# Kernel tuning notes

Hardware: AMD Instinct MI355X
Metric: run time of the kernel (lower is better)

Reference implementation:

```python
import jax, jax.numpy as jnp
import numpy as np

N_PTS = 2000   # n: number of Z1 samples (rows of K_Z1Z1)
Z_PTS = 2000   # z: number of Z2 samples (cols of K_Z1Z2 / gammas)
A_SAMP = 1000  # a: number of alpha samples
D = 8          # d: treatment dimension


def setup_inputs() -> dict:
    key = jax.random.key(0)
    ks = jax.random.split(key, 8)
    M = jax.random.normal(ks[0], (N_PTS, D), jnp.float32)
    N = jax.random.normal(ks[1], (N_PTS, D), jnp.float32)
    X = (M + N) / 2  # initial_X in the torch module (the nn.Parameter)
    # PSD kernel matrix so the ridge solve is well conditioned
    A = jax.random.normal(ks[2], (N_PTS, N_PTS), jnp.float32)
    K_Z1Z1 = (A @ A.T) / N_PTS
    K_Z1Z2 = jax.random.normal(ks[3], (N_PTS, Z_PTS), jnp.float32) * 0.1
    gamma_MN = jax.random.normal(ks[4], (N_PTS, Z_PTS), jnp.float32) * 0.01
    # offset keeps the complex denominator exps @ gamma_N away from zero
    gamma_N = jax.random.normal(ks[5], (N_PTS, Z_PTS), jnp.float32) * 0.01 + 1.0 / N_PTS
    alpha_samples = jax.random.normal(ks[6], (A_SAMP, D), jnp.float32)
    log_lambda_X = jnp.zeros((1,), jnp.float32)  # log(lambda_N) with lambda_N = 1.0
    return {
        "M": M, "N": N, "X": X, "log_lambda_X": log_lambda_X,
        "K_Z1Z1": K_Z1Z1, "K_Z1Z2": K_Z1Z2,
        "gamma_MN": gamma_MN, "gamma_N": gamma_N,
        "alpha_samples": alpha_samples,
    }


def _compute_labels(alpha, exponent, gamma_num, gamma_den, mult_num):
    # exps: [a, n] complex64 phase features exp(i * <alpha, exponent_j>)
    exps = jnp.exp(1j * (alpha @ exponent.T))
    # denominator: [a, z]
    denom = exps @ gamma_den.astype(jnp.complex64)
    # numerator: [a, z, d]
    num = jnp.einsum('jd,jz,aj->azd',
                     mult_num.astype(jnp.complex64),
                     gamma_num.astype(jnp.complex64),
                     exps)
    return num / denom[:, :, None]


def reference(M, N, X, log_lambda_X, K_Z1Z1, K_Z1Z2, gamma_MN, gamma_N, alpha_samples):
    n = K_Z1Z1.shape[0]
    # kernel ridge solve: gamma_X = (K + n*exp(log_lambda)*I)^{-1} K_Z1Z2  -> [n, z]
    reg = n * jnp.exp(log_lambda_X[0])
    gamma_X = jnp.linalg.solve(K_Z1Z1 + reg * jnp.eye(n, dtype=K_Z1Z1.dtype), K_Z1Z2)
    MN_labels = _compute_labels(alpha_samples, N, gamma_MN, gamma_N, M)   # [a, z, d]
    X_labels = _compute_labels(alpha_samples, X, gamma_X, gamma_X, X)     # [a, z, d]
    diff = MN_labels - X_labels
    # torch.linalg.norm(., dim=-1)**2 on complex == sum |.|^2 over d
    loss = jnp.mean(jnp.sum(jnp.abs(diff) ** 2, axis=-1))
    return loss
```

## Files before the change

### kernel.cpp

```cpp
#include <hip/hip_runtime.h>


typedef __bf16 bf16;
typedef __bf16 bf16x8 __attribute__((ext_vector_type(8)));
typedef float f32x4 __attribute__((ext_vector_type(4)));
typedef int i32x8 __attribute__((ext_vector_type(8)));
typedef int i32x4 __attribute__((ext_vector_type(4)));

#define AS1 __attribute__((address_space(1)))
#define AS3 __attribute__((address_space(3)))

__device__ __forceinline__ void async16(const void* g, void* l) {
  __builtin_amdgcn_global_load_lds((AS1 const unsigned int*)g,
                                   (AS3 unsigned int*)l, 16, 0, 0);
}

__device__ __forceinline__ unsigned int pk4f8(float a, float b, float c,
                                              float d) {
  int w = __builtin_amdgcn_cvt_pk_fp8_f32(a, b, 0, false);
  w = __builtin_amdgcn_cvt_pk_fp8_f32(c, d, w, true);
  return (unsigned int)w;
}

__device__ __forceinline__ i32x8 ld_swz32(const unsigned char* rowp, int kg,
                                          int fsw) {
  i32x4 lo = *(const i32x4*)(rowp + (kg ^ fsw));
  i32x4 hi = *(const i32x4*)(rowp + ((kg + 16) ^ fsw));
  i32x8 v;
  v[0] = lo[0]; v[1] = lo[1]; v[2] = lo[2]; v[3] = lo[3];
  v[4] = hi[0]; v[5] = hi[1]; v[6] = hi[2]; v[7] = hi[3];
  return v;
}

__device__ __forceinline__ void stage64x64(const float* __restrict__ src,
                                           int row0, int col0,
                                           float (*t)[65], int tid) {
#pragma unroll
  for (int it = 0; it < 4; ++it) {
    int e = it * 256 + tid;
    int r = e >> 4, c4 = (e & 15) * 4;
    float4 v = {0.f, 0.f, 0.f, 0.f};
    if (row0 + r < 2000 && col0 + c4 < 2000)
      v = *(const float4*)(src + (size_t)(row0 + r) * 2000 + col0 + c4);
    t[r][c4] = v.x; t[r][c4 + 1] = v.y; t[r][c4 + 2] = v.z; t[r][c4 + 3] = v.w;
  }
}

__device__ __forceinline__ void build_mn(const float* __restrict__ gMN,
                                         const float* __restrict__ Mm,
                                         unsigned char* __restrict__ B8,
                                         int j0, int zl0, int zg0, int ZC,
                                         int tid, float (*t)[65]) {
  const size_t PL = (size_t)ZC * 2048;
  int zg = zg0 + zl0;
  stage64x64(gMN, j0, zg, t, tid);
  __syncthreads();
  const float4* M4 = (const float4*)Mm;
#pragma unroll
  for (int it = 0; it < 2; ++it) {
    int idx = it * 256 + tid;
    int zr = idx >> 3, c8 = (idx & 7) * 8;
    float g[8], mrow[8][8];
#pragma unroll
    for (int e = 0; e < 8; ++e) {
      g[e] = 64.f * t[c8 + e][zr];
      int jj = j0 + c8 + e;
      if (jj < 2000) {
        float4 ma = M4[jj * 2], mb = M4[jj * 2 + 1];
        mrow[e][0] = ma.x; mrow[e][1] = ma.y; mrow[e][2] = ma.z;
        mrow[e][3] = ma.w; mrow[e][4] = mb.x; mrow[e][5] = mb.y;
        mrow[e][6] = mb.z; mrow[e][7] = mb.w;
      } else {
#pragma unroll
        for (int d = 0; d < 8; ++d) mrow[e][d] = 0.f;
      }
    }
    size_t ob = (size_t)(zl0 + zr) * 2048 + j0 + c8;
#pragma unroll
    for (int d = 0; d < 8; ++d) {
      uint2 u;
      u.x = pk4f8(g[0] * mrow[0][d], g[1] * mrow[1][d], g[2] * mrow[2][d],
                  g[3] * mrow[3][d]);
      u.y = pk4f8(g[4] * mrow[4][d], g[5] * mrow[5][d], g[6] * mrow[6][d],
                  g[7] * mrow[7][d]);
      *(uint2*)(B8 + (size_t)d * PL + ob) = u;
    }
  }
}

__device__ __forceinline__ void build_x(const bf16* __restrict__ gxHi,
                                        const bf16* __restrict__ gxLo,
                                        const float* __restrict__ Xm,
                                        unsigned char* __restrict__ B8,
                                        int j0, int zl0, int zg0, int ZC,
                                        int tid) {
  const size_t PL = (size_t)ZC * 2048;
  const float4* X4 = (const float4*)Xm;
#pragma unroll
  for (int it = 0; it < 2; ++it) {
    int idx = it * 256 + tid;
    int zr = idx >> 3, c8 = (idx & 7) * 8;
    size_t gb = (size_t)(zg0 + zl0 + zr) * 2048 + j0 + c8;
    bf16x8 vh = *(const bf16x8*)(gxHi + gb);
    bf16x8 vl = *(const bf16x8*)(gxLo + gb);
    float gx[8], xr[8][8];
#pragma unroll
    for (int e = 0; e < 8; ++e) {
      gx[e] = 8192.f * ((float)vh[e] + (float)vl[e]);
      int jj = j0 + c8 + e;
      if (jj < 2000) {
        float4 xa = X4[jj * 2], xb = X4[jj * 2 + 1];
        xr[e][0] = xa.x; xr[e][1] = xa.y; xr[e][2] = xa.z; xr[e][3] = xa.w;
        xr[e][4] = xb.x; xr[e][5] = xb.y; xr[e][6] = xb.z; xr[e][7] = xb.w;
      } else {
#pragma unroll
        for (int d = 0; d < 8; ++d) xr[e][d] = 0.f;
      }
    }
    size_t ob = (size_t)(zl0 + zr) * 2048 + j0 + c8;
#pragma unroll
    for (int d = 0; d < 8; ++d) {
      uint2 u;
      u.x = pk4f8(gx[0] * xr[0][d], gx[1] * xr[1][d], gx[2] * xr[2][d],
                  gx[3] * xr[3][d]);
      u.y = pk4f8(gx[4] * xr[4][d], gx[5] * xr[5][d], gx[6] * xr[6][d],
                  gx[7] * xr[7][d]);
      *(uint2*)(B8 + (size_t)(8 + d) * PL + ob) = u;
    }
  }
}

__global__ __launch_bounds__(256) void k_cvt(
    const float* __restrict__ K11, const float* __restrict__ K12,
    const float* __restrict__ gN, bf16* __restrict__ Kbf,
    bf16* __restrict__ K12T, bf16* __restrict__ K12TL,
    bf16* __restrict__ BtNh, bf16* __restrict__ BtNl,
    float* __restrict__ out) {
  __shared__ float t[64][65];
  const int bid = blockIdx.x, tid = threadIdx.x;
  if (bid < 2048) {
    if (bid == 0 && tid == 0) out[0] = 0.f;
    int e = (bid * 256 + tid) * 8;
    int j = e >> 11, k = e & 2047;
    bf16x8 v;
    if (j < 2000 && k < 2000) {
      const float4* s = (const float4*)(K11 + (size_t)j * 2000 + k);
      float4 f0 = s[0], f1 = s[1];
      v[0] = (bf16)f0.x; v[1] = (bf16)f0.y; v[2] = (bf16)f0.z; v[3] = (bf16)f0.w;
      v[4] = (bf16)f1.x; v[5] = (bf16)f1.y; v[6] = (bf16)f1.z; v[7] = (bf16)f1.w;
    } else {
      for (int i = 0; i < 8; ++i) v[i] = (bf16)0.f;
    }
    *(bf16x8*)(Kbf + e) = v;
  } else {
    bool isK12 = bid < 3072;
    const float* src = isK12 ? K12 : gN;
    bf16* dh = isK12 ? K12T : BtNh;
    bf16* dl = isK12 ? K12TL : BtNl;
    int b2 = bid - (isK12 ? 2048 : 3072);
    int j0 = (b2 & 31) * 64, z0 = (b2 >> 5) * 64;
    stage64x64(src, j0, z0, t, tid);
    __syncthreads();
#pragma unroll
    for (int it = 0; it < 2; ++it) {
      int idx = it * 256 + tid;
      int zr = idx >> 3, c8 = (idx & 7) * 8;
      bf16x8 vh, vl;
#pragma unroll
      for (int e = 0; e < 8; ++e) {
        float g = t[c8 + e][zr];
        bf16 h = (bf16)g;
        vh[e] = h;
        vl[e] = (bf16)(g - (float)h);
      }
      size_t ob = (size_t)(z0 + zr) * 2048 + j0 + c8;
      *(bf16x8*)(dh + ob) = vh;
      *(bf16x8*)(dl + ob) = vl;
    }
  }
}

__global__ __launch_bounds__(256, 2) void k_big(
    const bf16* __restrict__ K12T, const bf16* __restrict__ K12TL,
    const bf16* __restrict__ Kbf, const float* __restrict__ ll,
    const float* __restrict__ al, const float* __restrict__ Nm,
    const float* __restrict__ Xm, const float* __restrict__ gMN,
    const float* __restrict__ Mm, bf16* __restrict__ gxHi,
    bf16* __restrict__ gxLo, bf16* __restrict__ AphH,
    bf16* __restrict__ AphL, unsigned char* __restrict__ Aph8,
    unsigned char* __restrict__ B8, int ZC) {
  __shared__ __align__(16) char smem[34816];
  const int tid = threadIdx.x;
  const int bid = blockIdx.x;
  if (bid >= 1280) {
    int pid = bid - 1280;
    build_mn(gMN, Mm, B8, (pid & 31) * 64, (pid >> 5) * 64, 0, ZC, tid,
             (float(*)[65])smem);
    return;
  }
  if (bid >= 256) {
    const size_t PA = (size_t)1024 * 2048;
    int a = bid - 256;
    int j0 = tid * 8;
    float vc[4][8];
    if (a < 1000) {
      const float4* A4 = (const float4*)al;
      const float4* N4 = (const float4*)Nm;
      const float4* X4 = (const float4*)Xm;
      float4 a0 = A4[a * 2], a1 = A4[a * 2 + 1];
#pragma unroll
      for (int e = 0; e < 8; ++e) {
        int j = j0 + e;
        if (j < 2000) {
          float4 n0 = N4[j * 2], n1 = N4[j * 2 + 1];
          float4 x0 = X4[j * 2], x1 = X4[j * 2 + 1];
          float pn = a0.x * n0.x + a0.y * n0.y + a0.z * n0.z + a0.w * n0.w +
                     a1.x * n1.x + a1.y * n1.y + a1.z * n1.z + a1.w * n1.w;
          float px = a0.x * x0.x + a0.y * x0.y + a0.z * x0.z + a0.w * x0.w +
                     a1.x * x1.x + a1.y * x1.y + a1.z * x1.z + a1.w * x1.w;
          __sincosf(pn, &vc[1][e], &vc[0][e]);
          __sincosf(px, &vc[3][e], &vc[2][e]);
        } else {
          vc[0][e] = vc[1][e] = vc[2][e] = vc[3][e] = 0.f;
        }
      }
    } else {
#pragma unroll
      for (int p = 0; p < 4; ++p)
#pragma unroll
        for (int e = 0; e < 8; ++e) vc[p][e] = 0.f;
    }
    size_t o = (size_t)a * 2048 + j0;
#pragma unroll
    for (int p = 0; p < 4; ++p) {
      bf16x8 vh, vl;
#pragma unroll
      for (int e = 0; e < 8; ++e) {
        bf16 h = (bf16)vc[p][e];
        vh[e] = h;
        vl[e] = (bf16)(vc[p][e] - (float)h);
      }
      *(bf16x8*)(AphH + p * PA + o) = vh;
      *(bf16x8*)(AphL + p * PA + o) = vl;
      uint2 u8;
      u8.x = pk4f8(vc[p][0], vc[p][1], vc[p][2], vc[p][3]);
      u8.y = pk4f8(vc[p][4], vc[p][5], vc[p][6], vc[p][7]);
      *(uint2*)(Aph8 + p * PA + o) = u8;
    }
    return;
  }
  bf16(*lds)[128][64] = (bf16(*)[128][64])smem;
  int wrk = (bid & 7) * 32 + (bid >> 3);
  int bm = (wrk >> 4) * 128;
  int bn = (wrk & 15) * 128;
  const int w = tid >> 6, ln = tid & 63;
  const int r8 = ln >> 3, c8 = (ln & 7) * 8;
  f32x4 acc[4][4];
#pragma unroll
  for (int i = 0; i < 4; i++)
#pragma unroll
    for (int j = 0; j < 4; j++) acc[i][j] = {0.f, 0.f, 0.f, 0.f};
  const int m0 = (w & 1) * 64, n0 = (w >> 1) * 64;
  const int fr = ln & 15, kq = (ln >> 4) * 8;
  const int esw = (fr & 7) << 3;
  for (int kt = 0; kt < 2048; kt += 64) {
#pragma unroll
    for (int q = 0; q < 4; ++q) {
      int row = (w * 4 + q) * 8 + r8;
      int sc = c8 ^ ((row & 7) << 3);
      async16(K12T + (size_t)(bm + row) * 2048 + (kt + sc), &lds[0][row][c8]);
      async16(Kbf + (size_t)(bn + row) * 2048 + (kt + sc), &lds[1][row][c8]);
    }
    __syncthreads();
#pragma unroll
    for (int ks = 0; ks < 64; ks += 32) {
      bf16x8 a[4], b[4];
#pragma unroll
      for (int i = 0; i < 4; i++) {
        a[i] = *(const bf16x8*)&lds[0][m0 + i * 16 + fr][(ks + kq) ^ esw];
        b[i] = *(const bf16x8*)&lds[1][n0 + i * 16 + fr][(ks + kq) ^ esw];
      }
      __builtin_amdgcn_s_setprio(1);
#pragma unroll
      for (int i = 0; i < 4; i++)
#pragma unroll
        for (int j = 0; j < 4; j++)
          acc[i][j] = __builtin_amdgcn_mfma_f32_16x16x32_bf16(
              a[i], b[j], acc[i][j], 0, 0, 0);
      __builtin_amdgcn_s_setprio(0);
    }
    __syncthreads();
  }
  float inv = 1.f / (2000.f * __expf(ll[0]));
  float* ft = (float*)smem;
  const int cr = (ln >> 4) * 4, cc = ln & 15;
  const int gtid = (tid & 7) * 8;
#pragma unroll
  for (int h = 0; h < 2; ++h) {
    if ((w >> 1) == h) {
#pragma unroll
      for (int i = 0; i < 4; i++)
#pragma unroll
        for (int j = 0; j < 4; j++)
#pragma unroll
          for (int r = 0; r < 4; r++)
            ft[(m0 + i * 16 + cr + r) * 68 + j * 16 + cc] = acc[i][j][r];
    }
    __syncthreads();
    int jbase = bn + h * 64 + gtid;
#pragma unroll
    for (int it = 0; it < 4; ++it) {
      int idx = it * 256 + tid;
      int m = idx >> 3;
      int zg = bm + m;
      size_t gb = (size_t)zg * 2048 + jbase;
      bf16x8 kh = *(const bf16x8*)(K12T + gb);
      bf16x8 klo = *(const bf16x8*)(K12TL + gb);
      bf16x8 vh, vl;
#pragma unroll
      for (int e = 0; e < 8; ++e) {
        float t1 = ft[m * 68 + gtid + e];
        float gx = ((float)kh[e] + (float)klo[e] - t1 * inv) * inv;
        bf16 hh = (bf16)gx;
        vh[e] = hh;
        vl[e] = (bf16)(gx - (float)hh);
      }
      *(bf16x8*)(gxHi + gb) = vh;
      *(bf16x8*)(gxLo + gb) = vl;
    }
    __syncthreads();
  }
}

__global__ __launch_bounds__(256) void k_prepX(
    const bf16* __restrict__ gxHi, const bf16* __restrict__ gxLo,
    const float* __restrict__ Xm, unsigned char* __restrict__ B8, int ZC) {
  int pid = blockIdx.x;
  build_x(gxHi, gxLo, Xm, B8, (pid & 31) * 64, (pid >> 5) * 64, 0, ZC,
          threadIdx.x);
}

__global__ __launch_bounds__(256, 2) void k_mm(
    const bf16* __restrict__ AphH, const bf16* __restrict__ AphL,
    const unsigned char* __restrict__ Aph8,
    const unsigned char* __restrict__ B8, const bf16* __restrict__ BtNh,
    const bf16* __restrict__ BtNl, const bf16* __restrict__ gxHi,
    const bf16* __restrict__ gxLo, unsigned int* __restrict__ Cpk,
    float* __restrict__ den, int ZC, int zg0) {
  const size_t PA = (size_t)1024 * 2048;
  const size_t PL8 = (size_t)ZC * 2048;
  const size_t PC = (size_t)1024 * ZC;
  __shared__ __align__(16) bf16 smem[3 * 128 * 64];
  const int tid = threadIdx.x;
  const int w = tid >> 6, ln = tid & 63;
  const int fr = ln & 15;
  const int cr = (ln >> 4) * 4, cc = ln & 15;

  const int BYT = ZC >> 7;
  const int nyT = ZC >> 6;
  const int xcd = blockIdx.x & 7;
  const int slot = blockIdx.x >> 3;
  const int numSlots = 16 * BYT;

  if (slot < numSlots) {
    const int half = numSlots >> 1;
    int zb = xcd * 2 + (slot >= half ? 1 : 0);
    int rem = slot & (half - 1);
    int bn = (rem >> 3) * 128;
    int bm = (rem & 7) * 128;

    unsigned char* l8 = (unsigned char*)smem;
    const unsigned char* A0 = Aph8 + (size_t)(zb < 8 ? 0 : 2) * PA;
    const unsigned char* A1 = A0 + PA;
    const unsigned char* B = B8 + (size_t)zb * PL8;
    const int sb = (zb < 8) ? 0x79797979 : 0x72727272;
    unsigned int* P = Cpk + (size_t)zb * PC;
    const int colb = (ln & 7) * 16;
    const int kg = (ln >> 4) * 32;
    const int fsw = (fr & 7) << 4;

    f32x4 acc0[4][4], acc1[4][4];
#pragma unroll
    for (int i = 0; i < 4; i++)
#pragma unroll
      for (int j = 0; j < 4; j++) {
        acc0[i][j] = {0.f, 0.f, 0.f, 0.f};
        acc1[i][j] = {0.f, 0.f, 0.f, 0.f};
      }
    const int m0 = (w & 1) * 64, n0 = (w >> 1) * 64;

    for (int kt = 0; kt < 2048; kt += 128) {
#pragma unroll
      for (int q = 0; q < 4; ++q) {
        int row = w * 32 + q * 8 + (ln >> 3);
        int sc = colb ^ ((row & 7) << 4);
        async16(A0 + (size_t)(bm + row) * 2048 + kt + sc,
                l8 + row * 128 + colb);
        async16(A1 + (size_t)(bm + row) * 2048 + kt + sc,
                l8 + 16384 + row * 128 + colb);
        async16(B + (size_t)(bn + row) * 2048 + kt + sc,
                l8 + 32768 + row * 128 + colb);
      }
      __syncthreads();
      i32x8 a0[4], a1[4];
#pragma unroll
      for (int i = 0; i < 4; i++) {
        const unsigned char* pr = l8 + (m0 + i * 16 + fr) * 128;
        a0[i] = ld_swz32(pr, kg, fsw);
        a1[i] = ld_swz32(pr + 16384, kg, fsw);
      }
      __builtin_amdgcn_s_setprio(1);
#pragma unroll
      for (int j = 0; j < 4; ++j) {
        i32x8 bfv =
            ld_swz32(l8 + 32768 + (n0 + j * 16 + fr) * 128, kg, fsw);
#pragma unroll
        for (int i = 0; i < 4; ++i) {
          acc0[i][j] = __builtin_amdgcn_mfma_scale_f32_16x16x128_f8f6f4(
              a0[i], bfv, acc0[i][j], 0, 0, 0, 0x7F7F7F7F, 0, sb);
          acc1[i][j] = __builtin_amdgcn_mfma_scale_f32_16x16x128_f8f6f4(
              a1[i], bfv, acc1[i][j], 0, 0, 0, 0x7F7F7F7F, 0, sb);
        }
      }
      __builtin_amdgcn_s_setprio(0);
      __syncthreads();
    }
#pragma unroll
    for (int i = 0; i < 4; i++)
#pragma unroll
      for (int j = 0; j < 4; j++)
#pragma unroll
        for (int r = 0; r < 4; r++) {
          union { bf16 h[2]; unsigned int u; } pk;
          pk.h[0] = (bf16)acc0[i][j][r];
          pk.h[1] = (bf16)acc1[i][j][r];
          P[(size_t)(bm + m0 + i * 16 + cr + r) * ZC +
            (bn + n0 + j * 16 + cc)] = pk.u;
        }
  } else {
    bf16(*lds)[64] = (bf16(*)[64])smem;
    const int kq = (ln >> 4) * 8;
    const int esw = (fr & 7) << 3;
    int j = slot - numSlots;
    int p = xcd >> 1;
    int ny = (xcd & 1) * (nyT >> 1) + (j >> 3);
    int side = p >> 1, trig = p & 1;
    const bf16* Ah = AphH + (size_t)(side * 2 + trig) * PA;
    const bf16* Al = AphL + (size_t)(side * 2 + trig) * PA;
    const bf16* Bh = (side ? gxHi : BtNh) + (size_t)zg0 * 2048;
    const bf16* Bl = (side ? gxLo : BtNl) + (size_t)zg0 * 2048;
    float* C = den + (size_t)p * PC;
    int bm = (j & 7) * 128, bn = ny * 64;
    const int r32 = tid >> 3, c8 = (tid & 7) * 8;

    f32x4 acc[4][2];
#pragma unroll
    for (int i = 0; i < 4; i++)
#pragma unroll
      for (int jj = 0; jj < 2; jj++) acc[i][jj] = {0.f, 0.f, 0.f, 0.f};
    const int m0 = (w & 1) * 64, n0 = (w >> 1) * 32;

    for (int kt = 0; kt < 2048; kt += 64) {
#pragma unroll
      for (int q = 0; q < 4; ++q) {
        int row = q * 32 + r32;
        int sc = c8 ^ ((row & 7) << 3);
        async16(Ah + (size_t)(bm + row) * 2048 + (kt + sc), &lds[row][c8]);
        async16(Al + (size_t)(bm + row) * 2048 + (kt + sc),
                &lds[128 + row][c8]);
      }
#pragma unroll
      for (int q = 0; q < 2; ++q) {
        int row = q * 32 + r32;
        int sc = c8 ^ ((row & 7) << 3);
        async16(Bh + (size_t)(bn + row) * 2048 + (kt + sc),
                &lds[256 + row][c8]);
        async16(Bl + (size_t)(bn + row) * 2048 + (kt + sc),
                &lds[320 + row][c8]);
      }
      __syncthreads();
#pragma unroll
      for (int ks = 0; ks < 64; ks += 32) {
        bf16x8 ah[4], alo[4], bh[2], blo[2];
#pragma unroll
        for (int i = 0; i < 4; i++) {
          ah[i]  = *(const bf16x8*)&lds[m0 + i * 16 + fr][(ks + kq) ^ esw];
          alo[i] =
              *(const bf16x8*)&lds[128 + m0 + i * 16 + fr][(ks + kq) ^ esw];
        }
#pragma unroll
        for (int jj = 0; jj < 2; jj++) {
          bh[jj] =
              *(const bf16x8*)&lds[256 + n0 + jj * 16 + fr][(ks + kq) ^ esw];
          blo[jj] =
              *(const bf16x8*)&lds[320 + n0 + jj * 16 + fr][(ks + kq) ^ esw];
        }
        __builtin_amdgcn_s_setprio(1);
#pragma unroll
        for (int i = 0; i < 4; i++)
#pragma unroll
          for (int jj = 0; jj < 2; jj++) {
            acc[i][jj] = __builtin_amdgcn_mfma_f32_16x16x32_bf16(
                alo[i], bh[jj], acc[i][jj], 0, 0, 0);
            acc[i][jj] = __builtin_amdgcn_mfma_f32_16x16x32_bf16(
                ah[i], blo[jj], acc[i][jj], 0, 0, 0);
            acc[i][jj] = __builtin_amdgcn_mfma_f32_16x16x32_bf16(
                ah[i], bh[jj], acc[i][jj], 0, 0, 0);
          }
        __builtin_amdgcn_s_setprio(0);
      }
      __syncthreads();
    }
#pragma unroll
    for (int i = 0; i < 4; i++)
#pragma unroll
      for (int jj = 0; jj < 2; jj++)
#pragma unroll
        for (int r = 0; r < 4; r++) {
          size_t idx = (size_t)(bm + m0 + i * 16 + cr + r) * ZC +
                       (bn + n0 + jj * 16 + cc);
          C[idx] = acc[i][jj][r];
        }
  }
}

__device__ __forceinline__ void load8p(const unsigned int* p, float* re,
                                       float* im) {
  uint4 u0 = ((const uint4*)p)[0], u1 = ((const uint4*)p)[1];
  re[0] = __uint_as_float(u0.x << 16); im[0] = __uint_as_float(u0.x & 0xffff0000u);
  re[1] = __uint_as_float(u0.y << 16); im[1] = __uint_as_float(u0.y & 0xffff0000u);
  re[2] = __uint_as_float(u0.z << 16); im[2] = __uint_as_float(u0.z & 0xffff0000u);
  re[3] = __uint_as_float(u0.w << 16); im[3] = __uint_as_float(u0.w & 0xffff0000u);
  re[4] = __uint_as_float(u1.x << 16); im[4] = __uint_as_float(u1.x & 0xffff0000u);
  re[5] = __uint_as_float(u1.y << 16); im[5] = __uint_as_float(u1.y & 0xffff0000u);
  re[6] = __uint_as_float(u1.z << 16); im[6] = __uint_as_float(u1.z & 0xffff0000u);
  re[7] = __uint_as_float(u1.w << 16); im[7] = __uint_as_float(u1.w & 0xffff0000u);
}
__device__ __forceinline__ void load8d(const float* p, float* o) {
  float4 f0 = ((const float4*)p)[0], f1 = ((const float4*)p)[1];
  o[0] = f0.x; o[1] = f0.y; o[2] = f0.z; o[3] = f0.w;
  o[4] = f1.x; o[5] = f1.y; o[6] = f1.z; o[7] = f1.w;
}

__global__ __launch_bounds__(256) void k_redprep(
    const unsigned int* __restrict__ Cpk, const float* __restrict__ den,
    float* __restrict__ out, const float* __restrict__ gMN,
    const float* __restrict__ Mm, const bf16* __restrict__ gxHi,
    const bf16* __restrict__ gxLo, const float* __restrict__ Xm,
    unsigned char* __restrict__ B8Next, int ZC, int zg0) {
  __shared__ float sm[64][65];
  const int bid = blockIdx.x, tid = threadIdx.x;
  if (bid >= 1000) {
    int pid = bid - 1000;
    int j0 = (pid & 31) * 64, zl0 = (pid >> 5) * 64;
    int zg0n = zg0 + ZC;
    build_mn(gMN, Mm, B8Next, j0, zl0, zg0n, ZC, tid, sm);
    build_x(gxHi, gxLo, Xm, B8Next, j0, zl0, zg0n, ZC, tid);
    return;
  }
  const size_t PS = (size_t)1024 * ZC;
  const int a = bid;
  float acc = 0.f;
  for (int z = tid * 8; z < ZC; z += 2048) {
    if (zg0 + z >= 2000) break;
    size_t base = (size_t)a * ZC + z;
    float mdr[8], mdi[8], xdr[8], xdi[8], im[8], ix[8];
    load8d(den + 0 * PS + base, mdr);
    load8d(den + 1 * PS + base, mdi);
    load8d(den + 2 * PS + base, xdr);
    load8d(den + 3 * PS + base, xdi);
#pragma unroll
    for (int e = 0; e < 8; ++e) {
      im[e] = 1.f / (mdr[e] * mdr[e] + mdi[e] * mdi[e]);
      ix[e] = 1.f / (xdr[e] * xdr[e] + xdi[e] * xdi[e]);
    }
#pragma unroll
    for (int d = 0; d < 8; ++d) {
      float ar[8], ai[8], br[8], bi[8];
      load8p(Cpk + (size_t)d * PS + base, ar, ai);
      load8p(Cpk + (size_t)(8 + d) * PS + base, br, bi);
#pragma unroll
      for (int e = 0; e < 8; ++e) {
        float r1 = (ar[e] * mdr[e] + ai[e] * mdi[e]) * im[e];
        float i1 = (ai[e] * mdr[e] - ar[e] * mdi[e]) * im[e];
        float r2 = (br[e] * xdr[e] + bi[e] * xdi[e]) * ix[e];
        float i2 = (bi[e] * xdr[e] - br[e] * xdi[e]) * ix[e];
        float dr = r1 - r2, di = i1 - i2;
        acc += dr * dr + di * di;
      }
    }
  }
  for (int off = 32; off; off >>= 1) acc += __shfl_down(acc, off, 64);
  __shared__ float red[4];
  if (!(tid & 63)) red[tid >> 6] = acc;
  __syncthreads();
  if (!tid)
    atomicAdd(out, (red[0] + red[1] + red[2] + red[3]) * (1.f / 2000000.f));
}

extern "C" void kernel_launch(void* const* d_in, const int* in_sizes, int n_in,
                              void* d_out, int out_size, void* d_ws,
                              size_t ws_size, hipStream_t stream) {
  const float* Mm  = (const float*)d_in[0];
  const float* Nm  = (const float*)d_in[1];
  const float* Xm  = (const float*)d_in[2];
  const float* ll  = (const float*)d_in[3];
  const float* K11 = (const float*)d_in[4];
  const float* K12 = (const float*)d_in[5];
  const float* gMN = (const float*)d_in[6];
  const float* gN  = (const float*)d_in[7];
  const float* al  = (const float*)d_in[8];

  char* ws = (char*)d_ws;
  const size_t MB = 1024 * 1024;
  bf16* AphH = (bf16*)(ws);
  bf16* AphL = (bf16*)(ws + 16 * MB);
  unsigned char* Aph8 = (unsigned char*)(ws + 32 * MB);
  bf16* gxHi = (bf16*)(ws + 40 * MB);
  bf16* gxLo = (bf16*)(ws + 48 * MB);
  bf16* BtNh = (bf16*)(ws + 56 * MB);
  bf16* BtNl = (bf16*)(ws + 64 * MB);
  char* chunkRgn = ws + 72 * MB;

  size_t fixedNeed = 96 * MB;
  size_t avail = (ws_size > fixedNeed) ? ws_size - fixedNeed : 0;
  int ZC = 2048;
  while (ZC > 128 && (size_t)114688 * ZC > avail) ZC >>= 1;
  int NC = 2048 / ZC;
  unsigned char* B8c = (unsigned char*)(chunkRgn);
  float* denc = (float*)(chunkRgn + (size_t)32768 * ZC);
  unsigned int* Cpkc = (unsigned int*)(chunkRgn + (size_t)49152 * ZC);
  char* trans = chunkRgn + (size_t)114688 * ZC;
  bf16* Kbf   = (bf16*)(trans);
  bf16* K12T  = (bf16*)(trans + 8 * MB);
  bf16* K12TL = (bf16*)(trans + 16 * MB);

  int NBP = 32 * (ZC / 64);
  int GMM = 192 * (ZC >> 7);

  k_cvt<<<dim3(4096), dim3(256), 0, stream>>>(K11, K12, gN, Kbf, K12T, K12TL,
                                              BtNh, BtNl, (float*)d_out);
  k_big<<<dim3(1280 + NBP), dim3(256), 0, stream>>>(
      K12T, K12TL, Kbf, ll, al, Nm, Xm, gMN, Mm, gxHi, gxLo, AphH, AphL, Aph8,
      B8c, ZC);
  k_prepX<<<dim3(NBP), dim3(256), 0, stream>>>(gxHi, gxLo, Xm, B8c, ZC);
  for (int c = 0; c < NC; ++c) {
    int zg0 = c * ZC;
    k_mm<<<dim3(GMM), dim3(256), 0, stream>>>(
        AphH, AphL, Aph8, B8c, BtNh, BtNl, gxHi, gxLo, Cpkc, denc, ZC, zg0);
    int nblk = (c + 1 < NC) ? 1000 + NBP : 1000;
    k_redprep<<<dim3(nblk), dim3(256), 0, stream>>>(
        Cpkc, denc, (float*)d_out, gMN, Mm, gxHi, gxLo, Xm, B8c, ZC, zg0);
  }
  (void)in_sizes; (void)n_in; (void)out_size;
}
```

Measured before the change: 467.3 us.

## Halve GEMM tile width in k_big and pack two alpha rows per redprep block

The gamma_X GEMM section of k_big moves from 128x128 tiles (256 blocks) to 128x64 tiles (512 blocks), so more blocks are in flight across the CUs and the epilogue needs only one LDS staging pass instead of two. The trade is lower data reuse per tile, since the A operand is now loaded twice as often. k_redprep now gives each block two alpha rows with 128 threads each, halving the block count for the reduction part. All block-index offsets and launch sizes are updated to match.

Result: faster. 448.9 us (-3.9%).

```diff
diff --git a/kernel.cpp b/kernel.cpp
--- a/kernel.cpp
+++ b/kernel.cpp
@@ -192,15 +192,15 @@
   __shared__ __align__(16) char smem[34816];
   const int tid = threadIdx.x;
   const int bid = blockIdx.x;
-  if (bid >= 1280) {
-    int pid = bid - 1280;
+  if (bid >= 1536) {
+    int pid = bid - 1536;
     build_mn(gMN, Mm, B8, (pid & 31) * 64, (pid >> 5) * 64, 0, ZC, tid,
              (float(*)[65])smem);
     return;
   }
-  if (bid >= 256) {
+  if (bid >= 512) {
     const size_t PA = (size_t)1024 * 2048;
-    int a = bid - 256;
+    int a = bid - 512;
     int j0 = tid * 8;
     float vc[4][8];
     if (a < 1000) {
@@ -249,44 +249,51 @@
     }
     return;
   }
-  bf16(*lds)[128][64] = (bf16(*)[128][64])smem;
-  int wrk = (bid & 7) * 32 + (bid >> 3);
-  int bm = (wrk >> 4) * 128;
-  int bn = (wrk & 15) * 128;
+  bf16(*lds)[64] = (bf16(*)[64])smem;
+  int wrk = (bid & 7) * 64 + (bid >> 3);
+  int bm = (wrk >> 5) * 128;
+  int bn = (wrk & 31) * 64;
   const int w = tid >> 6, ln = tid & 63;
-  const int r8 = ln >> 3, c8 = (ln & 7) * 8;
-  f32x4 acc[4][4];
-#pragma unroll
-  for (int i = 0; i < 4; i++)
-#pragma unroll
-    for (int j = 0; j < 4; j++) acc[i][j] = {0.f, 0.f, 0.f, 0.f};
-  const int m0 = (w & 1) * 64, n0 = (w >> 1) * 64;
   const int fr = ln & 15, kq = (ln >> 4) * 8;
   const int esw = (fr & 7) << 3;
+  const int r32 = tid >> 3, c8 = (tid & 7) * 8;
+  f32x4 acc[4][2];
+#pragma unroll
+  for (int i = 0; i < 4; i++)
+#pragma unroll
+    for (int jj = 0; jj < 2; jj++) acc[i][jj] = {0.f, 0.f, 0.f, 0.f};
+  const int m0 = (w & 1) * 64, n0 = (w >> 1) * 32;
   for (int kt = 0; kt < 2048; kt += 64) {
 #pragma unroll
     for (int q = 0; q < 4; ++q) {
-      int row = (w * 4 + q) * 8 + r8;
+      int row = q * 32 + r32;
       int sc = c8 ^ ((row & 7) << 3);
-      async16(K12T + (size_t)(bm + row) * 2048 + (kt + sc), &lds[0][row][c8]);
-      async16(Kbf + (size_t)(bn + row) * 2048 + (kt + sc), &lds[1][row][c8]);
+      async16(K12T + (size_t)(bm + row) * 2048 + (kt + sc), &lds[row][c8]);
+    }
+#pragma unroll
+    for (int q = 0; q < 2; ++q) {
+      int row = q * 32 + r32;
+      int sc = c8 ^ ((row & 7) << 3);
+      async16(Kbf + (size_t)(bn + row) * 2048 + (kt + sc),
+              &lds[128 + row][c8]);
     }
     __syncthreads();
 #pragma unroll
     for (int ks = 0; ks < 64; ks += 32) {
-      bf16x8 a[4], b[4];
-#pragma unroll
-      for (int i = 0; i < 4; i++) {
-        a[i] = *(const bf16x8*)&lds[0][m0 + i * 16 + fr][(ks + kq) ^ esw];
-        b[i] = *(const bf16x8*)&lds[1][n0 + i * 16 + fr][(ks + kq) ^ esw];
-      }
+      bf16x8 a[4], b[2];
+#pragma unroll
+      for (int i = 0; i < 4; i++)
+        a[i] = *(const bf16x8*)&lds[m0 + i * 16 + fr][(ks + kq) ^ esw];
+#pragma unroll
+      for (int jj = 0; jj < 2; jj++)
+        b[jj] = *(const bf16x8*)&lds[128 + n0 + jj * 16 + fr][(ks + kq) ^ esw];
       __builtin_amdgcn_s_setprio(1);
 #pragma unroll
       for (int i = 0; i < 4; i++)
 #pragma unroll
-        for (int j = 0; j < 4; j++)
-          acc[i][j] = __builtin_amdgcn_mfma_f32_16x16x32_bf16(
-              a[i], b[j], acc[i][j], 0, 0, 0);
+        for (int jj = 0; jj < 2; jj++)
+          acc[i][jj] = __builtin_amdgcn_mfma_f32_16x16x32_bf16(
+              a[i], b[jj], acc[i][jj], 0, 0, 0);
       __builtin_amdgcn_s_setprio(0);
     }
     __syncthreads();
@@ -294,41 +301,32 @@
   float inv = 1.f / (2000.f * __expf(ll[0]));
   float* ft = (float*)smem;
   const int cr = (ln >> 4) * 4, cc = ln & 15;
-  const int gtid = (tid & 7) * 8;
-#pragma unroll
-  for (int h = 0; h < 2; ++h) {
-    if ((w >> 1) == h) {
-#pragma unroll
-      for (int i = 0; i < 4; i++)
-#pragma unroll
-        for (int j = 0; j < 4; j++)
-#pragma unroll
-          for (int r = 0; r < 4; r++)
-            ft[(m0 + i * 16 + cr + r) * 68 + j * 16 + cc] = acc[i][j][r];
-    }
-    __syncthreads();
-    int jbase = bn + h * 64 + gtid;
-#pragma unroll
-    for (int it = 0; it < 4; ++it) {
-      int idx = it * 256 + tid;
-      int m = idx >> 3;
-      int zg = bm + m;
-      size_t gb = (size_t)zg * 2048 + jbase;
-      bf16x8 kh = *(const bf16x8*)(K12T + gb);
-      bf16x8 klo = *(const bf16x8*)(K12TL + gb);
-      bf16x8 vh, vl;
-#pragma unroll
-      for (int e = 0; e < 8; ++e) {
-        float t1 = ft[m * 68 + gtid + e];
-        float gx = ((float)kh[e] + (float)klo[e] - t1 * inv) * inv;
-        bf16 hh = (bf16)gx;
-        vh[e] = hh;
-        vl[e] = (bf16)(gx - (float)hh);
-      }
-      *(bf16x8*)(gxHi + gb) = vh;
-      *(bf16x8*)(gxLo + gb) = vl;
-    }
-    __syncthreads();
+#pragma unroll
+  for (int i = 0; i < 4; i++)
+#pragma unroll
+    for (int jj = 0; jj < 2; jj++)
+#pragma unroll
+      for (int r = 0; r < 4; r++)
+        ft[(m0 + i * 16 + cr + r) * 66 + n0 + jj * 16 + cc] = acc[i][jj][r];
+  __syncthreads();
+#pragma unroll
+  for (int it = 0; it < 4; ++it) {
+    int idx = it * 256 + tid;
+    int m = idx >> 3, cg = (idx & 7) * 8;
+    size_t gb = (size_t)(bm + m) * 2048 + bn + cg;
+    bf16x8 kh = *(const bf16x8*)(K12T + gb);
+    bf16x8 klo = *(const bf16x8*)(K12TL + gb);
+    bf16x8 vh, vl;
+#pragma unroll
+    for (int e = 0; e < 8; ++e) {
+      float t1 = ft[m * 66 + cg + e];
+      float gx = ((float)kh[e] + (float)klo[e] - t1 * inv) * inv;
+      bf16 hh = (bf16)gx;
+      vh[e] = hh;
+      vl[e] = (bf16)(gx - (float)hh);
+    }
+    *(bf16x8*)(gxHi + gb) = vh;
+    *(bf16x8*)(gxLo + gb) = vl;
   }
 }
 
@@ -550,8 +548,8 @@
     unsigned char* __restrict__ B8Next, int ZC, int zg0) {
   __shared__ float sm[64][65];
   const int bid = blockIdx.x, tid = threadIdx.x;
-  if (bid >= 1000) {
-    int pid = bid - 1000;
+  if (bid >= 500) {
+    int pid = bid - 500;
     int j0 = (pid & 31) * 64, zl0 = (pid >> 5) * 64;
     int zg0n = zg0 + ZC;
     build_mn(gMN, Mm, B8Next, j0, zl0, zg0n, ZC, tid, sm);
@@ -559,9 +557,10 @@
     return;
   }
   const size_t PS = (size_t)1024 * ZC;
-  const int a = bid;
+  int a = bid * 2 + (tid >> 7);
+  int zt = tid & 127;
   float acc = 0.f;
-  for (int z = tid * 8; z < ZC; z += 2048) {
+  for (int z = zt * 8; z < ZC; z += 1024) {
     if (zg0 + z >= 2000) break;
     size_t base = (size_t)a * ZC + z;
     float mdr[8], mdi[8], xdr[8], xdi[8], im[8], ix[8];
@@ -640,7 +639,7 @@
 
   k_cvt<<<dim3(4096), dim3(256), 0, stream>>>(K11, K12, gN, Kbf, K12T, K12TL,
                                               BtNh, BtNl, (float*)d_out);
-  k_big<<<dim3(1280 + NBP), dim3(256), 0, stream>>>(
+  k_big<<<dim3(1536 + NBP), dim3(256), 0, stream>>>(
       K12T, K12TL, Kbf, ll, al, Nm, Xm, gMN, Mm, gxHi, gxLo, AphH, AphL, Aph8,
       B8c, ZC);
   k_prepX<<<dim3(NBP), dim3(256), 0, stream>>>(gxHi, gxLo, Xm, B8c, ZC);
@@ -648,7 +647,7 @@
     int zg0 = c * ZC;
     k_mm<<<dim3(GMM), dim3(256), 0, stream>>>(
         AphH, AphL, Aph8, B8c, BtNh, BtNl, gxHi, gxLo, Cpkc, denc, ZC, zg0);
-    int nblk = (c + 1 < NC) ? 1000 + NBP : 1000;
+    int nblk = (c + 1 < NC) ? 500 + NBP : 500;
     k_redprep<<<dim3(nblk), dim3(256), 0, stream>>>(
         Cpkc, denc, (float*)d_out, gMN, Mm, gxHi, gxLo, Xm, B8c, ZC, zg0);
   }
```
